# Kernel optimization log

Hardware: AMD Instinct MI355X
Metric: run time of the kernel (lower is better)

The kernel has to match this reference:

```python
import jax, jax.numpy as jnp
import numpy as np

B, WORDS, DIM = 16, 32, 256
HEADS, DIM_HEAD = 8, 32
INNER = HEADS * DIM_HEAD  # 256 == DIM -> project_out True
ITER = 3
J = WORDS * HEADS  # input capsules axis


def setup_inputs() -> dict:
    key = jax.random.key(0)
    ks = jax.random.split(key, 6)
    x = jax.random.normal(ks[0], (B, WORDS, DIM), jnp.float32)
    # capsule transform weights: [J, I, E, D] = [words*heads, words, inner, dim_head]
    W = jax.random.normal(ks[1], (J, WORDS, INNER, DIM_HEAD), jnp.float32)
    bias = 0.01 * jax.random.normal(ks[2], (J, WORDS, INNER), jnp.float32)
    Wi = jax.random.normal(ks[3], (INNER, DIM), jnp.float32) / np.sqrt(DIM)
    bi = jnp.zeros((INNER,), jnp.float32)
    Wo = jax.random.normal(ks[4], (DIM, INNER), jnp.float32) / np.sqrt(INNER)
    bo = jnp.zeros((DIM,), jnp.float32)
    return {"x": x, "W": W, "bias": bias, "Wi": Wi, "bi": bi, "Wo": Wo, "bo": bo}


def _squash(s):
    n = jnp.linalg.norm(s, axis=-1, keepdims=True)
    return n / (1.0 + n * n) * s


def reference(x, W, bias, Wi, bi, Wo, bo):
    # inner projection: [B, WORDS, INNER]
    xi = x @ Wi.T + bi
    # 'b n (h d) -> b (n h) d'
    xh = xi.reshape(B, WORDS * HEADS, DIM_HEAD)
    # u_hat[b,j,i,e] = sum_d W[j,i,e,d] * xh[b,j,d]  -> [B, J, WORDS, INNER]
    u_hat = jnp.einsum('jied,bjd->bjie', W, xh) + bias
    u_det = jax.lax.stop_gradient(u_hat)
    b_log = jnp.zeros_like(u_hat)
    v = None
    for i in range(ITER):
        c = jax.nn.softmax(b_log, axis=2)          # over output capsules (words)
        u = u_hat if i == ITER - 1 else u_det       # detach except last iter
        s = jnp.sum(c * u, axis=1, keepdims=True)   # [B,1,WORDS,INNER]
        v = _squash(s)
        if i < ITER - 1:
            b_log = b_log + jnp.sum(u_det * v, axis=3, keepdims=True)
    out = jnp.squeeze(v, 1) @ Wo.T + bo             # [B, WORDS, DIM]
    return out
```

## Files before the change

kernel.cpp:

```cpp
#include <hip/hip_runtime.h>

#define BB   16
#define NW   32
#define DIMM 256
#define DH   32
#define NI   256
#define NJ   256

__global__ void k_proj_in(const float* __restrict__ x, const float* __restrict__ Wi,
                          const float* __restrict__ bi, float* __restrict__ xh) {
    int row = blockIdx.x;
    int k = threadIdx.x;
    __shared__ float xr[DIMM];
    xr[k] = x[(size_t)row * DIMM + k];
    __syncthreads();
    const float4* wi  = (const float4*)(Wi + (size_t)k * DIMM);
    const float4* xr4 = (const float4*)xr;
    float acc = bi[k];
#pragma unroll 8
    for (int m = 0; m < DIMM / 4; ++m) {
        float4 w = wi[m]; float4 xv = xr4[m];
        acc += w.x * xv.x + w.y * xv.y + w.z * xv.z + w.w * xv.w;
    }
    xh[(size_t)row * DIMM + k] = acc;
}

__global__ void k_uhat(const float* __restrict__ W, const float* __restrict__ bias,
                       const float* __restrict__ xh, float* __restrict__ u) {
    int j = blockIdx.x >> 5;
    int i = blockIdx.x & 31;
    int e = threadIdx.x;
    __shared__ float xs[BB][DH];
    for (int t = threadIdx.x; t < BB * DH; t += 256) {
        int b = t >> 5, d = t & 31;
        xs[b][d] = xh[((size_t)b * NJ + j) * DH + d];
    }
    __syncthreads();
    const float4* wp = (const float4*)(W + (((size_t)j * NW + i) * NI + e) * DH);
    float4 w4[8];
#pragma unroll
    for (int q = 0; q < 8; ++q) w4[q] = wp[q];
    const float* w = (const float*)w4;
    float bv = bias[((size_t)j * NW + i) * NI + e];
    for (int b = 0; b < BB; ++b) {
        float acc = bv;
#pragma unroll
        for (int d = 0; d < DH; ++d) acc += w[d] * xs[b][d];
        u[(((size_t)b * NJ + j) * NW + i) * NI + e] = acc;
    }
}

__global__ void k_beta(const float* __restrict__ u, const float* __restrict__ v,
                       float* __restrict__ b_log, float* __restrict__ c, int accflag) {
    int b = blockIdx.x >> 8;
    int j = blockIdx.x & 255;
    int tid = threadIdx.x;
    int lane = tid & 63, wave = tid >> 6;
    const float* up = u + ((size_t)b * NJ + j) * NW * NI;
    const float* vp = v + (size_t)b * NW * NI;
    __shared__ float red[NW][4];
    for (int row = 0; row < NW; ++row) {
        float p = up[(size_t)row * NI + tid] * vp[(size_t)row * NI + tid];
#pragma unroll
        for (int off = 32; off >= 1; off >>= 1) p += __shfl_down(p, off);
        if (lane == 0) red[row][wave] = p;
    }
    __syncthreads();
    if (tid < NW) {
        float bta = red[tid][0] + red[tid][1] + red[tid][2] + red[tid][3];
        size_t bidx = ((size_t)b * NJ + j) * NW + tid;
        if (accflag) bta += b_log[bidx];
        b_log[bidx] = bta;
        float m = bta;
#pragma unroll
        for (int mask = 16; mask >= 1; mask >>= 1) m = fmaxf(m, __shfl_xor(m, mask));
        float ex = __expf(bta - m);
        float s = ex;
#pragma unroll
        for (int mask = 16; mask >= 1; mask >>= 1) s += __shfl_xor(s, mask);
        c[bidx] = ex / s;
    }
}

__global__ void k_sum_squash(const float* __restrict__ u, const float* __restrict__ c,
                             float* __restrict__ v, int uniform) {
    int b = blockIdx.x >> 5;
    int i = blockIdx.x & 31;
    int tid = threadIdx.x;
    int lane = tid & 63, wave = tid >> 6;
    __shared__ float cs[NJ];
    __shared__ float red[4];
    if (uniform) cs[tid] = 1.0f / NW;
    else         cs[tid] = c[((size_t)b * NJ + tid) * NW + i];
    __syncthreads();
    float acc = 0.f;
    const float* up = u + ((size_t)b * NJ * NW + i) * NI + tid;
#pragma unroll 4
    for (int j = 0; j < NJ; ++j) acc += cs[j] * up[(size_t)j * NW * NI];
    float p = acc * acc;
#pragma unroll
    for (int off = 32; off >= 1; off >>= 1) p += __shfl_down(p, off);
    if (lane == 0) red[wave] = p;
    __syncthreads();
    float n2 = red[0] + red[1] + red[2] + red[3];
    float n = sqrtf(n2);
    float f = n / (1.0f + n2);
    v[((size_t)b * NW + i) * NI + tid] = f * acc;
}

__global__ void k_proj_out(const float* __restrict__ v, const float* __restrict__ Wo,
                           const float* __restrict__ bo, float* __restrict__ out) {
    int row = blockIdx.x;
    int k = threadIdx.x;
    __shared__ float vr[NI];
    vr[k] = v[(size_t)row * NI + k];
    __syncthreads();
    const float4* wo  = (const float4*)(Wo + (size_t)k * NI);
    const float4* vr4 = (const float4*)vr;
    float acc = bo[k];
#pragma unroll 8
    for (int m = 0; m < NI / 4; ++m) {
        float4 w = wo[m]; float4 xv = vr4[m];
        acc += w.x * xv.x + w.y * xv.y + w.z * xv.z + w.w * xv.w;
    }
    out[(size_t)row * DIMM + k] = acc;
}

extern "C" void kernel_launch(void* const* d_in, const int* in_sizes, int n_in,
                              void* d_out, int out_size, void* d_ws, size_t ws_size,
                              hipStream_t stream) {
    const float* x    = (const float*)d_in[0];
    const float* W    = (const float*)d_in[1];
    const float* bias = (const float*)d_in[2];
    const float* Wi   = (const float*)d_in[3];
    const float* bi   = (const float*)d_in[4];
    const float* Wo   = (const float*)d_in[5];
    const float* bo   = (const float*)d_in[6];
    float* out = (float*)d_out;

    float* ws    = (float*)d_ws;
    float* xh    = ws;
    float* u     = ws + 131072;
    float* b_log = u + 33554432;
    float* c     = b_log + 131072;
    float* v     = c + 131072;

    k_proj_in<<<dim3(BB * NW), dim3(256), 0, stream>>>(x, Wi, bi, xh);
    k_uhat<<<dim3(NJ * NW), dim3(256), 0, stream>>>(W, bias, xh, u);

    k_sum_squash<<<dim3(BB * NW), dim3(256), 0, stream>>>(u, nullptr, v, 1);
    k_beta<<<dim3(BB * NJ), dim3(256), 0, stream>>>(u, v, b_log, c, 0);
    k_sum_squash<<<dim3(BB * NW), dim3(256), 0, stream>>>(u, c, v, 0);
    k_beta<<<dim3(BB * NJ), dim3(256), 0, stream>>>(u, v, b_log, c, 1);
    k_sum_squash<<<dim3(BB * NW), dim3(256), 0, stream>>>(u, c, v, 0);

    k_proj_out<<<dim3(BB * NW), dim3(256), 0, stream>>>(v, Wo, bo, out);
}
```

Before: 604.8 us.

## Fuse routing softmax with weighted capsule sum using per-group partial sums

The separate beta/softmax and weighted-sum kernels are merged into one routing kernel. It processes a group of 8 input capsules per block, computes agreement and softmax, and accumulates the c·u partial sums from the same u values held in registers. The u-hat kernel also emits uniform-weight partial sums, so the first sum pass no longer rereads u. A small reduce kernel then combines the partials and applies squash. This cuts the number of passes over the large u tensor. In exchange, grids are much smaller and each thread carries heavy register arrays, so latency hiding may suffer.

```diff
diff --git a/kernel.cpp b/kernel.cpp
--- a/kernel.cpp
+++ b/kernel.cpp
@@ -6,6 +6,8 @@
 #define DH   32
 #define NI   256
 #define NJ   256
+#define JP   8
+#define JG   (NJ / JP)
 
 __global__ void k_proj_in(const float* __restrict__ x, const float* __restrict__ Wi,
                           const float* __restrict__ bi, float* __restrict__ xh) {
@@ -26,77 +28,110 @@
 }
 
 __global__ void k_uhat(const float* __restrict__ W, const float* __restrict__ bias,
-                       const float* __restrict__ xh, float* __restrict__ u) {
-    int j = blockIdx.x >> 5;
-    int i = blockIdx.x & 31;
-    int e = threadIdx.x;
+                       const float* __restrict__ xh, float* __restrict__ u,
+                       float* __restrict__ part) {
+    int jg = blockIdx.x >> 5;
+    int i  = blockIdx.x & 31;
+    int e  = threadIdx.x;
     __shared__ float xs[BB][DH];
-    for (int t = threadIdx.x; t < BB * DH; t += 256) {
-        int b = t >> 5, d = t & 31;
-        xs[b][d] = xh[((size_t)b * NJ + j) * DH + d];
+    float acc0[BB];
+#pragma unroll
+    for (int b = 0; b < BB; ++b) acc0[b] = 0.f;
+
+    for (int jj = 0; jj < JP; ++jj) {
+        int j = jg * JP + jj;
+        __syncthreads();
+        for (int t = threadIdx.x; t < BB * DH; t += 256) {
+            int b = t >> 5, d = t & 31;
+            xs[b][d] = xh[((size_t)b * NJ + j) * DH + d];
+        }
+        __syncthreads();
+        const float4* wp = (const float4*)(W + (((size_t)j * NW + i) * NI + e) * DH);
+        float4 w4[8];
+#pragma unroll
+        for (int q = 0; q < 8; ++q) w4[q] = wp[q];
+        const float* w = (const float*)w4;
+        float bv = bias[((size_t)j * NW + i) * NI + e];
+#pragma unroll
+        for (int b = 0; b < BB; ++b) {
+            float a = bv;
+#pragma unroll
+            for (int d = 0; d < DH; ++d) a += w[d] * xs[b][d];
+            u[(((size_t)b * NJ + j) * NW + i) * NI + e] = a;
+            acc0[b] += a;
+        }
     }
-    __syncthreads();
-    const float4* wp = (const float4*)(W + (((size_t)j * NW + i) * NI + e) * DH);
-    float4 w4[8];
 #pragma unroll
-    for (int q = 0; q < 8; ++q) w4[q] = wp[q];
-    const float* w = (const float*)w4;
-    float bv = bias[((size_t)j * NW + i) * NI + e];
-    for (int b = 0; b < BB; ++b) {
-        float acc = bv;
-#pragma unroll
-        for (int d = 0; d < DH; ++d) acc += w[d] * xs[b][d];
-        u[(((size_t)b * NJ + j) * NW + i) * NI + e] = acc;
-    }
+    for (int b = 0; b < BB; ++b)
+        part[(((size_t)b * JG + jg) * NW + i) * NI + e] = acc0[b];
 }
 
-__global__ void k_beta(const float* __restrict__ u, const float* __restrict__ v,
-                       float* __restrict__ b_log, float* __restrict__ c, int accflag) {
-    int b = blockIdx.x >> 8;
-    int j = blockIdx.x & 255;
+__global__ void k_route(const float* __restrict__ u, const float* __restrict__ v,
+                        float* __restrict__ b_log, float* __restrict__ part, int accflag) {
+    int b  = blockIdx.x / JG;
+    int jg = blockIdx.x % JG;
     int tid = threadIdx.x;
     int lane = tid & 63, wave = tid >> 6;
-    const float* up = u + ((size_t)b * NJ + j) * NW * NI;
-    const float* vp = v + (size_t)b * NW * NI;
+    __shared__ float vs[NW][NI];
     __shared__ float red[NW][4];
-    for (int row = 0; row < NW; ++row) {
-        float p = up[(size_t)row * NI + tid] * vp[(size_t)row * NI + tid];
+    __shared__ float cs[NW];
+    for (int t = tid; t < NW * NI; t += 256)
+        vs[t >> 8][t & 255] = v[(size_t)b * NW * NI + t];
+    __syncthreads();
+
+    float s_acc[NW];
 #pragma unroll
-        for (int off = 32; off >= 1; off >>= 1) p += __shfl_down(p, off);
-        if (lane == 0) red[row][wave] = p;
+    for (int i = 0; i < NW; ++i) s_acc[i] = 0.f;
+
+    for (int jj = 0; jj < JP; ++jj) {
+        int j = jg * JP + jj;
+        const float* up = u + ((size_t)b * NJ + j) * NW * NI;
+        float ur[NW];
+#pragma unroll
+        for (int i = 0; i < NW; ++i) ur[i] = up[(size_t)i * NI + tid];
+#pragma unroll
+        for (int i = 0; i < NW; ++i) {
+            float p = ur[i] * vs[i][tid];
+#pragma unroll
+            for (int off = 32; off >= 1; off >>= 1) p += __shfl_down(p, off);
+            if (lane == 0) red[i][wave] = p;
+        }
+        __syncthreads();
+        if (tid < NW) {
+            float bta = red[tid][0] + red[tid][1] + red[tid][2] + red[tid][3];
+            size_t bidx = ((size_t)b * NJ + j) * NW + tid;
+            if (accflag) bta += b_log[bidx];
+            b_log[bidx] = bta;
+            float m = bta;
+#pragma unroll
+            for (int mask = 16; mask >= 1; mask >>= 1) m = fmaxf(m, __shfl_xor(m, mask));
+            float ex = __expf(bta - m);
+            float ssum = ex;
+#pragma unroll
+            for (int mask = 16; mask >= 1; mask >>= 1) ssum += __shfl_xor(ssum, mask);
+            cs[tid] = ex / ssum;
+        }
+        __syncthreads();
+#pragma unroll
+        for (int i = 0; i < NW; ++i) s_acc[i] += cs[i] * ur[i];
     }
-    __syncthreads();
-    if (tid < NW) {
-        float bta = red[tid][0] + red[tid][1] + red[tid][2] + red[tid][3];
-        size_t bidx = ((size_t)b * NJ + j) * NW + tid;
-        if (accflag) bta += b_log[bidx];
-        b_log[bidx] = bta;
-        float m = bta;
 #pragma unroll
-        for (int mask = 16; mask >= 1; mask >>= 1) m = fmaxf(m, __shfl_xor(m, mask));
-        float ex = __expf(bta - m);
-        float s = ex;
-#pragma unroll
-        for (int mask = 16; mask >= 1; mask >>= 1) s += __shfl_xor(s, mask);
-        c[bidx] = ex / s;
-    }
+    for (int i = 0; i < NW; ++i)
+        part[(((size_t)b * JG + jg) * NW + i) * NI + tid] = s_acc[i];
 }
 
-__global__ void k_sum_squash(const float* __restrict__ u, const float* __restrict__ c,
-                             float* __restrict__ v, int uniform) {
+__global__ void k_reduce(const float* __restrict__ part, float* __restrict__ v,
+                         float scale) {
     int b = blockIdx.x >> 5;
     int i = blockIdx.x & 31;
     int tid = threadIdx.x;
     int lane = tid & 63, wave = tid >> 6;
-    __shared__ float cs[NJ];
+    float acc = 0.f;
+#pragma unroll 8
+    for (int g = 0; g < JG; ++g)
+        acc += part[(((size_t)b * JG + g) * NW + i) * NI + tid];
+    acc *= scale;
     __shared__ float red[4];
-    if (uniform) cs[tid] = 1.0f / NW;
-    else         cs[tid] = c[((size_t)b * NJ + tid) * NW + i];
-    __syncthreads();
-    float acc = 0.f;
-    const float* up = u + ((size_t)b * NJ * NW + i) * NI + tid;
-#pragma unroll 4
-    for (int j = 0; j < NJ; ++j) acc += cs[j] * up[(size_t)j * NW * NI];
     float p = acc * acc;
 #pragma unroll
     for (int off = 32; off >= 1; off >>= 1) p += __shfl_down(p, off);
@@ -141,18 +176,16 @@
     float* ws    = (float*)d_ws;
     float* xh    = ws;
     float* u     = ws + 131072;
-    float* b_log = u + 33554432;
-    float* c     = b_log + 131072;
-    float* v     = c + 131072;
+    float* part  = u + 33554432;
+    float* b_log = part + 4194304;
+    float* v     = b_log + 131072;
 
     k_proj_in<<<dim3(BB * NW), dim3(256), 0, stream>>>(x, Wi, bi, xh);
-    k_uhat<<<dim3(NJ * NW), dim3(256), 0, stream>>>(W, bias, xh, u);
-
-    k_sum_squash<<<dim3(BB * NW), dim3(256), 0, stream>>>(u, nullptr, v, 1);
-    k_beta<<<dim3(BB * NJ), dim3(256), 0, stream>>>(u, v, b_log, c, 0);
-    k_sum_squash<<<dim3(BB * NW), dim3(256), 0, stream>>>(u, c, v, 0);
-    k_beta<<<dim3(BB * NJ), dim3(256), 0, stream>>>(u, v, b_log, c, 1);
-    k_sum_squash<<<dim3(BB * NW), dim3(256), 0, stream>>>(u, c, v, 0);
-
+    k_uhat<<<dim3(JG * NW), dim3(256), 0, stream>>>(W, bias, xh, u, part);
+    k_reduce<<<dim3(BB * NW), dim3(256), 0, stream>>>(part, v, 1.0f / NW);
+    k_route<<<dim3(BB * JG), dim3(256), 0, stream>>>(u, v, b_log, part, 0);
+    k_reduce<<<dim3(BB * NW), dim3(256), 0, stream>>>(part, v, 1.0f);
+    k_route<<<dim3(BB * JG), dim3(256), 0, stream>>>(u, v, b_log, part, 1);
+    k_reduce<<<dim3(BB * NW), dim3(256), 0, stream>>>(part, v, 1.0f);
     k_proj_out<<<dim3(BB * NW), dim3(256), 0, stream>>>(v, Wo, bo, out);
 }
```

Measured after the change: 606.4 us. No clear change (+0.3%).
